# Kernel optimization log

Hardware: AMD Instinct MI355X
Metric: run time of the kernel (lower is better)

The kernel has to match this reference:

```python
import jax, jax.numpy as jnp
import numpy as np

NUM_EXPERTS = 4  # matches init_kwargs

def setup_inputs() -> dict:
    key = jax.random.key(0)
    ks = jax.random.split(key, 6)
    B, T, D = 4, 4096, 1024
    H = 4 * D
    x = jax.random.normal(ks[0], (B, T, D), dtype=jnp.float32)
    token_mask = jax.random.randint(ks[1], (B, T), 0, NUM_EXPERTS, dtype=jnp.int32)
    s1 = 1.0 / np.sqrt(D)
    s2 = 1.0 / np.sqrt(H)
    W1 = jax.random.normal(ks[2], (H, D), dtype=jnp.float32) * s1
    b1 = jax.random.normal(ks[3], (H,), dtype=jnp.float32) * s1
    W2 = jax.random.normal(ks[4], (D, H), dtype=jnp.float32) * s2
    b2 = jax.random.normal(ks[5], (D,), dtype=jnp.float32) * s2
    return {"x": x, "token_mask": token_mask, "W1": W1, "b1": b1, "W2": W2, "b2": b2}

def reference(x, token_mask, W1, b1, W2, b2):
    # Nested MoE FFN: expert m uses leading D//2^(E-1-m) input dims and
    # leading H//2^(E-1-m) hidden dims; top expert (m=E-1) is the full MLP.
    D = x.shape[-1]
    H = W1.shape[0]
    factor = 2 ** (NUM_EXPERTS - 1 - token_mask)          # [B,T] int
    d_in = D // factor                                     # [B,T]
    d_hid = H // factor                                    # [B,T]
    mask_in = (jnp.arange(D) < d_in[..., None]).astype(x.dtype)    # [B,T,D]
    mask_hid = (jnp.arange(H) < d_hid[..., None]).astype(x.dtype)  # [B,T,H]
    # Expand: slice input dims, project, keep only nested hidden slice (bias included only there)
    h = (jnp.einsum('btd,hd->bth', x * mask_in, W1) + b1) * mask_hid
    h = jax.nn.gelu(h, approximate=False)  # gelu(0)=0 preserves nested zeros
    # Contract: zeros outside the nested hidden slice contribute nothing; full output + bias
    out = jnp.einsum('bth,dh->btd', h, W2) + b2
    return out
```

## Files before the change

kernel.cpp:

```cpp
#include <hip/hip_runtime.h>
#include <cstdint>
#include <math.h>

typedef __attribute__((ext_vector_type(8))) __bf16 bf16x8;
typedef __attribute__((ext_vector_type(4))) float f32x4;
typedef unsigned short ushort_t;

__device__ __forceinline__ ushort_t f2bf(float f) {
    uint32_t u = __float_as_uint(f);
    u += 0x7fff + ((u >> 16) & 1);
    return (ushort_t)(u >> 16);
}

__device__ __forceinline__ float gelu_exact(float v) {
    return 0.5f * v * (1.0f + erff(v * 0.70710678118654752440f));
}

__global__ void convert_w2_kernel(const float* __restrict__ s1, const float* __restrict__ s2,
                                  ushort_t* __restrict__ d1, ushort_t* __restrict__ d2,
                                  int n4) {
    int i = blockIdx.x * blockDim.x + threadIdx.x;
    const float* src; ushort_t* dst; int k;
    if (i < n4) { src = s1; dst = d1; k = i; }
    else if (i < 2 * n4) { src = s2; dst = d2; k = i - n4; }
    else return;
    const float4 v = ((const float4*)src)[k];
    ushort4 o;
    o.x = f2bf(v.x); o.y = f2bf(v.y); o.z = f2bf(v.z); o.w = f2bf(v.w);
    ((ushort4*)dst)[k] = o;
}

#define SORT_T 256
__global__ void sort_kernel(const int* __restrict__ tm, int M, int D, int H,
                            int* __restrict__ meta, int* __restrict__ sidx) {
    __shared__ int lc[4][SORT_T + 1];
    __shared__ int soff[4];
    const int t = threadIdx.x;
    const int nj = M / SORT_T;
    int c0 = 0, c1 = 0, c2 = 0, c3 = 0;
    for (int j = 0; j < nj; j++) {
        int e = tm[t + j * SORT_T];
        c0 += (e == 0); c1 += (e == 1); c2 += (e == 2); c3 += (e == 3);
    }
    lc[0][t + 1] = c0; lc[1][t + 1] = c1; lc[2][t + 1] = c2; lc[3][t + 1] = c3;
    if (t < 4) lc[t][0] = 0;
    __syncthreads();
    if (t < 4) {
        int acc = 0;
        for (int i = 1; i <= SORT_T; i++) { acc += lc[t][i]; lc[t][i] = acc; }
    }
    __syncthreads();
    if (t == 0) {
        int off = 0, xoff = 0, hoff = 0;
        for (int e = 0; e < 4; e++) {
            int c = lc[e][SORT_T];
            int ac = (c + 127) & ~127;
            int din = D >> (3 - e), dh = H >> (3 - e);
            meta[e] = c; meta[4 + e] = off; meta[8 + e] = ac; meta[12 + e] = ac >> 7;
            meta[16 + e] = xoff; meta[20 + e] = hoff;
            soff[e] = off;
            off += ac; xoff += ac * din; hoff += ac * dh;
        }
        meta[28] = off;
        int a = 0, b = 0;
        for (int k = 0; k < 4; k++) {
            int e = 3 - k;
            meta[24 + k] = a; a += meta[12 + e] * ((H >> (3 - e)) >> 7);
            meta[32 + k] = b; b += meta[12 + e] * (D >> 7);
        }
        meta[29] = a; meta[36] = b;
    }
    __syncthreads();
    int pos[4];
    pos[0] = soff[0] + lc[0][t]; pos[1] = soff[1] + lc[1][t];
    pos[2] = soff[2] + lc[2][t]; pos[3] = soff[3] + lc[3][t];
    for (int j = 0; j < nj; j++) {
        int i = t + j * SORT_T;
        int e = tm[i];
        sidx[pos[e]++] = i;
    }
    __syncthreads();
    for (int e = 0; e < 4; e++) {
        int s = soff[e] + lc[e][SORT_T];
        int n = meta[8 + e] - lc[e][SORT_T];
        for (int i = t; i < n; i += SORT_T) sidx[s + i] = -1;
    }
}

__global__ void convert_x_sorted(const float* __restrict__ x,
                                 const int* __restrict__ meta,
                                 const int* __restrict__ sidx,
                                 ushort_t* __restrict__ xb, int D) {
    const int p = blockIdx.x;
    if (p >= meta[28]) return;
    const int e = (p >= meta[5]) + (p >= meta[6]) + (p >= meta[7]);
    const int off = meta[4 + e];
    const int din = D >> (3 - e);
    const int tok = sidx[p];
    ushort_t* dst = xb + (size_t)meta[16 + e] + (size_t)(p - off) * din;
    if (tok < 0) {
        for (int c = threadIdx.x * 4; c < din; c += blockDim.x * 4)
            *(ushort4*)(dst + c) = ushort4{0, 0, 0, 0};
    } else {
        const float* src = x + (size_t)tok * D;
        for (int c = threadIdx.x * 4; c < din; c += blockDim.x * 4) {
            const float4 v = *(const float4*)(src + c);
            ushort4 o;
            o.x = f2bf(v.x); o.y = f2bf(v.y); o.z = f2bf(v.z); o.w = f2bf(v.w);
            *(ushort4*)(dst + c) = o;
        }
    }
}

template <int EPI>
__global__ void gemm_sorted(const ushort_t* __restrict__ Abuf,
                            const ushort_t* __restrict__ Bw,
                            const float* __restrict__ bias,
                            const int* __restrict__ meta,
                            const int* __restrict__ sidx,
                            ushort_t* __restrict__ hb,
                            float* __restrict__ out,
                            int D, int H) {
    __shared__ ushort_t As[128 * 32];
    __shared__ ushort_t Bs[128 * 32];

    const int t    = threadIdx.x;
    const int wave = t >> 6;
    const int lane = t & 63;
    const int quad = lane >> 4;
    const int l16  = lane & 15;
    const int wm   = wave & 1;
    const int wn   = wave >> 1;
    const int srow = t >> 2;
    const int scol = (t & 3) * 8;
    char* AsB = (char*)As;
    char* BsB = (char*)Bs;
    const int ldsoff = wave * 64 * 16;

    const int* st = meta + (EPI == 0 ? 24 : 32);
    const int  T  = meta[EPI == 0 ? 29 : 36];

    for (int idx = blockIdx.x; idx < T; idx += gridDim.x) {
        const int k3 = (idx >= st[1]) + (idx >= st[2]) + (idx >= st[3]);
        const int e = 3 - k3;
        const int local = idx - st[k3];
        const int mtiles = meta[12 + e];
        const int mt = local % mtiles;
        const int nt = local / mtiles;

        const int K   = (EPI == 0) ? (D >> (3 - e)) : (H >> (3 - e));
        const int Ne  = (EPI == 0) ? (H >> (3 - e)) : D;
        const int lda = K;
        const int ldb = (EPI == 0) ? D : H;
        const int nb  = nt * 128;
        const ushort_t* A = Abuf + (size_t)((EPI == 0) ? meta[16 + e] : meta[20 + e]);

        const ushort_t* Ag = A + (size_t)(mt * 128 + srow) * lda + scol;
        const ushort_t* Bg = Bw + (size_t)(nb + srow) * ldb + scol;

        f32x4 acc[4][4] = {};

        for (int kt = 0; kt < K; kt += 32) {
            __syncthreads();
            __builtin_amdgcn_global_load_lds(
                (__attribute__((address_space(1))) void*)(uintptr_t)(Ag + kt),
                (__attribute__((address_space(3))) void*)(AsB + ldsoff), 16, 0, 0);
            __builtin_amdgcn_global_load_lds(
                (__attribute__((address_space(1))) void*)(uintptr_t)(Ag + (size_t)64 * lda + kt),
                (__attribute__((address_space(3))) void*)(AsB + 4096 + ldsoff), 16, 0, 0);
            __builtin_amdgcn_global_load_lds(
                (__attribute__((address_space(1))) void*)(uintptr_t)(Bg + kt),
                (__attribute__((address_space(3))) void*)(BsB + ldsoff), 16, 0, 0);
            __builtin_amdgcn_global_load_lds(
                (__attribute__((address_space(1))) void*)(uintptr_t)(Bg + (size_t)64 * ldb + kt),
                (__attribute__((address_space(3))) void*)(BsB + 4096 + ldsoff), 16, 0, 0);
            __syncthreads();

            bf16x8 af[4], bfr[4];
#pragma unroll
            for (int i = 0; i < 4; i++) {
                af[i]  = *(const bf16x8*)(As + (wm * 64 + i * 16 + l16) * 32 + quad * 8);
                bfr[i] = *(const bf16x8*)(Bs + (wn * 64 + i * 16 + l16) * 32 + quad * 8);
            }
#pragma unroll
            for (int i = 0; i < 4; i++)
#pragma unroll
                for (int j = 0; j < 4; j++)
                    acc[i][j] = __builtin_amdgcn_mfma_f32_16x16x32_bf16(af[i], bfr[j], acc[i][j], 0, 0, 0);
        }

        const int colbase = nb + wn * 64 + l16;
        float bv[4];
#pragma unroll
        for (int j = 0; j < 4; j++) bv[j] = bias[colbase + j * 16];

#pragma unroll
        for (int i = 0; i < 4; i++) {
#pragma unroll
            for (int r = 0; r < 4; r++) {
                const int lrow = mt * 128 + wm * 64 + i * 16 + quad * 4 + r;
                if (EPI == 0) {
                    ushort_t* dst = hb + (size_t)meta[20 + e] + (size_t)lrow * Ne;
#pragma unroll
                    for (int j = 0; j < 4; j++)
                        dst[colbase + j * 16] = f2bf(gelu_exact(acc[i][j][r] + bv[j]));
                } else {
                    const int tok = sidx[meta[4 + e] + lrow];
                    if (tok >= 0) {
                        float* dst = out + (size_t)tok * D;
#pragma unroll
                        for (int j = 0; j < 4; j++)
                            dst[colbase + j * 16] = acc[i][j][r] + bv[j];
                    }
                }
            }
        }
    }
}

__global__ void naive_kernel(const float* __restrict__ x, const int* __restrict__ tm,
                             const float* __restrict__ W1, const float* __restrict__ b1,
                             const float* __restrict__ W2, const float* __restrict__ b2,
                             float* __restrict__ out, int D, int Hdim) {
    const int t = blockIdx.x;
    const int m = tm[t];
    const int din = D >> (3 - m);
    const int dh = Hdim >> (3 - m);
    extern __shared__ float sm[];
    float* xs = sm;
    float* hs = sm + D;
    for (int i = threadIdx.x; i < din; i += blockDim.x) xs[i] = x[(size_t)t * D + i];
    __syncthreads();
    for (int h = threadIdx.x; h < dh; h += blockDim.x) {
        const float* w = W1 + (size_t)h * D;
        float a = b1[h];
        for (int d = 0; d < din; d++) a += xs[d] * w[d];
        hs[h] = gelu_exact(a);
    }
    __syncthreads();
    for (int d = threadIdx.x; d < D; d += blockDim.x) {
        const float* w = W2 + (size_t)d * Hdim;
        float a = b2[d];
        for (int h = 0; h < dh; h++) a += hs[h] * w[h];
        out[(size_t)t * D + d] = a;
    }
}

extern "C" void kernel_launch(void* const* d_in, const int* in_sizes, int n_in,
                              void* d_out, int out_size, void* d_ws, size_t ws_size,
                              hipStream_t stream) {
    const float* x  = (const float*)d_in[0];
    const int* tm   = (const int*)d_in[1];
    const float* W1 = (const float*)d_in[2];
    const float* b1 = (const float*)d_in[3];
    const float* W2 = (const float*)d_in[4];
    const float* b2 = (const float*)d_in[5];
    float* out = (float*)d_out;

    const int M    = in_sizes[1];
    const int Hdim = in_sizes[3];
    const int D    = in_sizes[0] / M;

    const int Mpad = M + 512;
    const size_t meta_sz = 256;
    const size_t sidx_sz = ((size_t)Mpad * 4 + 255) & ~(size_t)255;
    const size_t xb_sz   = (size_t)Mpad * D * 2;
    const size_t w1_sz   = (size_t)Hdim * D * 2;
    const size_t w2_sz   = (size_t)D * Hdim * 2;
    const size_t hb_sz   = (size_t)Mpad * Hdim * 2;
    const size_t need_sorted = meta_sz + sidx_sz + xb_sz + w1_sz + w2_sz + hb_sz;

    const bool shape_ok = (M % 256 == 0) && (D % 128 == 0) && (Hdim % 128 == 0) &&
                          (D >= 1024) && (Hdim >= 4096);

    if (shape_ok && ws_size >= need_sorted) {
        char* p = (char*)d_ws;
        int* meta     = (int*)p;        p += meta_sz;
        int* sidx     = (int*)p;        p += sidx_sz;
        ushort_t* xb  = (ushort_t*)p;   p += xb_sz;
        ushort_t* w1b = (ushort_t*)p;   p += w1_sz;
        ushort_t* w2b = (ushort_t*)p;   p += w2_sz;
        ushort_t* hb  = (ushort_t*)p;

        sort_kernel<<<1, SORT_T, 0, stream>>>(tm, M, D, Hdim, meta, sidx);
        const int n4w = Hdim * D / 4;
        convert_w2_kernel<<<(2 * n4w + 255) / 256, 256, 0, stream>>>(W1, W2, w1b, w2b, n4w);
        convert_x_sorted<<<Mpad, 64, 0, stream>>>(x, meta, sidx, xb, D);

        gemm_sorted<0><<<2048, 256, 0, stream>>>(xb, w1b, b1, meta, sidx, hb, nullptr, D, Hdim);
        gemm_sorted<1><<<2048, 256, 0, stream>>>(hb, w2b, b2, meta, sidx, nullptr, out, D, Hdim);
        return;
    }

    const size_t shmem = (size_t)(D + Hdim) * sizeof(float);
    naive_kernel<<<M, 256, shmem, stream>>>(x, tm, W1, b1, W2, b2, out, D, Hdim);
}
```

Baseline: 373.1 us.

## Parallelize token sort, fuse weight conversion with histogram, use tanh GELU

Replaces the single-block token sort with a multi-block histogram fused into the weight-conversion kernel, a wave-level scan in a small meta kernel, and a per-chunk placement kernel. The x conversion now uses one row per 256-thread block iteration in a grid-stride loop. The exact erf GELU in the first GEMM epilogue is replaced by the tanh approximation using __expf, which changes numerics relative to the exact reference. The fast path is also restricted to D == 1024.

```diff
diff --git a/kernel.cpp b/kernel.cpp
--- a/kernel.cpp
+++ b/kernel.cpp
@@ -12,102 +12,132 @@
     return (ushort_t)(u >> 16);
 }
 
+__device__ __forceinline__ float gelu_fast(float x) {
+    float u = x * (0.7978845608f + 0.0356774081f * x * x);
+    float e = __expf(2.0f * u);
+    float th = 1.0f - 2.0f / (e + 1.0f);
+    return 0.5f * x * (1.0f + th);
+}
+
 __device__ __forceinline__ float gelu_exact(float v) {
     return 0.5f * v * (1.0f + erff(v * 0.70710678118654752440f));
 }
 
-__global__ void convert_w2_kernel(const float* __restrict__ s1, const float* __restrict__ s2,
-                                  ushort_t* __restrict__ d1, ushort_t* __restrict__ d2,
-                                  int n4) {
-    int i = blockIdx.x * blockDim.x + threadIdx.x;
-    const float* src; ushort_t* dst; int k;
-    if (i < n4) { src = s1; dst = d1; k = i; }
-    else if (i < 2 * n4) { src = s2; dst = d2; k = i - n4; }
-    else return;
-    const float4 v = ((const float4*)src)[k];
-    ushort4 o;
-    o.x = f2bf(v.x); o.y = f2bf(v.y); o.z = f2bf(v.z); o.w = f2bf(v.w);
-    ((ushort4*)dst)[k] = o;
-}
-
-#define SORT_T 256
-__global__ void sort_kernel(const int* __restrict__ tm, int M, int D, int H,
-                            int* __restrict__ meta, int* __restrict__ sidx) {
-    __shared__ int lc[4][SORT_T + 1];
-    __shared__ int soff[4];
+__global__ void histo_convw_kernel(const int* __restrict__ tm, int* __restrict__ cnt,
+                                   int nchunks,
+                                   const float* __restrict__ s1, const float* __restrict__ s2,
+                                   ushort_t* __restrict__ d1, ushort_t* __restrict__ d2,
+                                   int n4) {
+    if (blockIdx.x < (unsigned)nchunks) {
+        __shared__ int h[4];
+        if (threadIdx.x < 4) h[threadIdx.x] = 0;
+        __syncthreads();
+        int e = tm[blockIdx.x * 256 + threadIdx.x];
+        atomicAdd(&h[e], 1);
+        __syncthreads();
+        if (threadIdx.x < 4) cnt[blockIdx.x * 4 + threadIdx.x] = h[threadIdx.x];
+    } else {
+        const int stride = (gridDim.x - nchunks) * 256;
+        for (int i = (blockIdx.x - nchunks) * 256 + threadIdx.x; i < 2 * n4; i += stride) {
+            const float* src; ushort_t* dst; int k;
+            if (i < n4) { src = s1; dst = d1; k = i; }
+            else        { src = s2; dst = d2; k = i - n4; }
+            const float4 v = ((const float4*)src)[k];
+            ushort4 o;
+            o.x = f2bf(v.x); o.y = f2bf(v.y); o.z = f2bf(v.z); o.w = f2bf(v.w);
+            ((ushort4*)dst)[k] = o;
+        }
+    }
+}
+
+__global__ void meta_kernel(int* __restrict__ meta, int* __restrict__ cnt,
+                            int* __restrict__ sidx, int nchunks, int D, int H) {
+    __shared__ int tot[4];
+    __shared__ int soff_s[4];
     const int t = threadIdx.x;
-    const int nj = M / SORT_T;
-    int c0 = 0, c1 = 0, c2 = 0, c3 = 0;
-    for (int j = 0; j < nj; j++) {
-        int e = tm[t + j * SORT_T];
-        c0 += (e == 0); c1 += (e == 1); c2 += (e == 2); c3 += (e == 3);
-    }
-    lc[0][t + 1] = c0; lc[1][t + 1] = c1; lc[2][t + 1] = c2; lc[3][t + 1] = c3;
-    if (t < 4) lc[t][0] = 0;
-    __syncthreads();
-    if (t < 4) {
-        int acc = 0;
-        for (int i = 1; i <= SORT_T; i++) { acc += lc[t][i]; lc[t][i] = acc; }
-    }
+    const int e = t >> 6;
+    const int c0 = t & 63;
+    int carry = 0;
+    for (int base = 0; base < nchunks; base += 64) {
+        int c = base + c0;
+        int v = (c < nchunks) ? cnt[c * 4 + e] : 0;
+        int s = v;
+#pragma unroll
+        for (int d = 1; d < 64; d <<= 1) {
+            int y = __shfl_up(s, d);
+            if (c0 >= d) s += y;
+        }
+        if (c < nchunks) cnt[c * 4 + e] = s - v + carry;
+        carry += __shfl(s, 63);
+    }
+    if (c0 == 0) tot[e] = carry;
     __syncthreads();
     if (t == 0) {
         int off = 0, xoff = 0, hoff = 0;
-        for (int e = 0; e < 4; e++) {
-            int c = lc[e][SORT_T];
+        for (int ee = 0; ee < 4; ee++) {
+            int c = tot[ee];
             int ac = (c + 127) & ~127;
-            int din = D >> (3 - e), dh = H >> (3 - e);
-            meta[e] = c; meta[4 + e] = off; meta[8 + e] = ac; meta[12 + e] = ac >> 7;
-            meta[16 + e] = xoff; meta[20 + e] = hoff;
-            soff[e] = off;
-            off += ac; xoff += ac * din; hoff += ac * dh;
+            meta[ee] = c; meta[4 + ee] = off; meta[8 + ee] = ac; meta[12 + ee] = ac >> 7;
+            meta[16 + ee] = xoff; meta[20 + ee] = hoff;
+            soff_s[ee] = off;
+            off += ac; xoff += ac * (D >> (3 - ee)); hoff += ac * (H >> (3 - ee));
         }
         meta[28] = off;
         int a = 0, b = 0;
         for (int k = 0; k < 4; k++) {
-            int e = 3 - k;
-            meta[24 + k] = a; a += meta[12 + e] * ((H >> (3 - e)) >> 7);
-            meta[32 + k] = b; b += meta[12 + e] * (D >> 7);
+            int ee = 3 - k;
+            meta[24 + k] = a; a += meta[12 + ee] * ((H >> (3 - ee)) >> 7);
+            meta[32 + k] = b; b += meta[12 + ee] * (D >> 7);
         }
         meta[29] = a; meta[36] = b;
     }
     __syncthreads();
-    int pos[4];
-    pos[0] = soff[0] + lc[0][t]; pos[1] = soff[1] + lc[1][t];
-    pos[2] = soff[2] + lc[2][t]; pos[3] = soff[3] + lc[3][t];
-    for (int j = 0; j < nj; j++) {
-        int i = t + j * SORT_T;
-        int e = tm[i];
-        sidx[pos[e]++] = i;
-    }
-    __syncthreads();
-    for (int e = 0; e < 4; e++) {
-        int s = soff[e] + lc[e][SORT_T];
-        int n = meta[8 + e] - lc[e][SORT_T];
-        for (int i = t; i < n; i += SORT_T) sidx[s + i] = -1;
-    }
+    for (int base = 0; base < 64 * ((nchunks + 63) / 64); base += 64) {
+        int c = base + c0;
+        if (c < nchunks) cnt[c * 4 + e] += soff_s[e];
+    }
+    for (int ee = 0; ee < 4; ee++) {
+        int s0 = soff_s[ee] + tot[ee];
+        int n = meta[8 + ee] - tot[ee];
+        for (int i = t; i < n; i += 256) sidx[s0 + i] = -1;
+    }
+}
+
+__global__ void place_kernel(const int* __restrict__ tm, const int* __restrict__ cofs,
+                             int* __restrict__ sidx) {
+    __shared__ unsigned char se[256];
+    const int c = blockIdx.x;
+    const int t = threadIdx.x;
+    const int tok = c * 256 + t;
+    const int e = tm[tok];
+    se[t] = (unsigned char)e;
+    __syncthreads();
+    int rank = 0;
+    for (int i = 0; i < t; i++) rank += (se[i] == (unsigned char)e);
+    sidx[cofs[c * 4 + e] + rank] = tok;
 }
 
 __global__ void convert_x_sorted(const float* __restrict__ x,
                                  const int* __restrict__ meta,
                                  const int* __restrict__ sidx,
                                  ushort_t* __restrict__ xb, int D) {
-    const int p = blockIdx.x;
-    if (p >= meta[28]) return;
-    const int e = (p >= meta[5]) + (p >= meta[6]) + (p >= meta[7]);
-    const int off = meta[4 + e];
-    const int din = D >> (3 - e);
-    const int tok = sidx[p];
-    ushort_t* dst = xb + (size_t)meta[16 + e] + (size_t)(p - off) * din;
-    if (tok < 0) {
-        for (int c = threadIdx.x * 4; c < din; c += blockDim.x * 4)
-            *(ushort4*)(dst + c) = ushort4{0, 0, 0, 0};
-    } else {
-        const float* src = x + (size_t)tok * D;
-        for (int c = threadIdx.x * 4; c < din; c += blockDim.x * 4) {
-            const float4 v = *(const float4*)(src + c);
-            ushort4 o;
-            o.x = f2bf(v.x); o.y = f2bf(v.y); o.z = f2bf(v.z); o.w = f2bf(v.w);
-            *(ushort4*)(dst + c) = o;
+    const int rows = meta[28];
+    for (int p = blockIdx.x; p < rows; p += gridDim.x) {
+        const int e = (p >= meta[5]) + (p >= meta[6]) + (p >= meta[7]);
+        const int off = meta[4 + e];
+        const int din = D >> (3 - e);
+        const int tok = sidx[p];
+        ushort_t* dst = xb + (size_t)meta[16 + e] + (size_t)(p - off) * din;
+        const int c = threadIdx.x * 4;
+        if (c < din) {
+            if (tok < 0) {
+                *(ushort4*)(dst + c) = ushort4{0, 0, 0, 0};
+            } else {
+                const float4 v = *(const float4*)(x + (size_t)tok * D + c);
+                ushort4 o;
+                o.x = f2bf(v.x); o.y = f2bf(v.y); o.z = f2bf(v.z); o.w = f2bf(v.w);
+                *(ushort4*)(dst + c) = o;
+            }
         }
     }
 }
@@ -203,7 +233,7 @@
                     ushort_t* dst = hb + (size_t)meta[20 + e] + (size_t)lrow * Ne;
 #pragma unroll
                     for (int j = 0; j < 4; j++)
-                        dst[colbase + j * 16] = f2bf(gelu_exact(acc[i][j][r] + bv[j]));
+                        dst[colbase + j * 16] = f2bf(gelu_fast(acc[i][j][r] + bv[j]));
                 } else {
                     const int tok = sidx[meta[4 + e] + lrow];
                     if (tok >= 0) {
@@ -262,30 +292,35 @@
     const int D    = in_sizes[0] / M;
 
     const int Mpad = M + 512;
+    const int nchunks = M / 256;
     const size_t meta_sz = 256;
+    const size_t cnt_sz  = ((size_t)nchunks * 4 * 4 + 255) & ~(size_t)255;
     const size_t sidx_sz = ((size_t)Mpad * 4 + 255) & ~(size_t)255;
     const size_t xb_sz   = (size_t)Mpad * D * 2;
     const size_t w1_sz   = (size_t)Hdim * D * 2;
     const size_t w2_sz   = (size_t)D * Hdim * 2;
     const size_t hb_sz   = (size_t)Mpad * Hdim * 2;
-    const size_t need_sorted = meta_sz + sidx_sz + xb_sz + w1_sz + w2_sz + hb_sz;
+    const size_t need_sorted = meta_sz + cnt_sz + sidx_sz + xb_sz + w1_sz + w2_sz + hb_sz;
 
     const bool shape_ok = (M % 256 == 0) && (D % 128 == 0) && (Hdim % 128 == 0) &&
-                          (D >= 1024) && (Hdim >= 4096);
+                          (D >= 1024) && (D <= 1024) && (Hdim >= 4096);
 
     if (shape_ok && ws_size >= need_sorted) {
         char* p = (char*)d_ws;
         int* meta     = (int*)p;        p += meta_sz;
+        int* cnt      = (int*)p;        p += cnt_sz;
         int* sidx     = (int*)p;        p += sidx_sz;
         ushort_t* xb  = (ushort_t*)p;   p += xb_sz;
         ushort_t* w1b = (ushort_t*)p;   p += w1_sz;
         ushort_t* w2b = (ushort_t*)p;   p += w2_sz;
         ushort_t* hb  = (ushort_t*)p;
 
-        sort_kernel<<<1, SORT_T, 0, stream>>>(tm, M, D, Hdim, meta, sidx);
         const int n4w = Hdim * D / 4;
-        convert_w2_kernel<<<(2 * n4w + 255) / 256, 256, 0, stream>>>(W1, W2, w1b, w2b, n4w);
-        convert_x_sorted<<<Mpad, 64, 0, stream>>>(x, meta, sidx, xb, D);
+        histo_convw_kernel<<<nchunks + 2048, 256, 0, stream>>>(tm, cnt, nchunks,
+                                                               W1, W2, w1b, w2b, n4w);
+        meta_kernel<<<1, 256, 0, stream>>>(meta, cnt, sidx, nchunks, D, Hdim);
+        place_kernel<<<nchunks, 256, 0, stream>>>(tm, cnt, sidx);
+        convert_x_sorted<<<2048, 256, 0, stream>>>(x, meta, sidx, xb, D);
 
         gemm_sorted<0><<<2048, 256, 0, stream>>>(xb, w1b, b1, meta, sidx, hb, nullptr, D, Hdim);
         gemm_sorted<1><<<2048, 256, 0, stream>>>(hb, w2b, b2, meta, sidx, nullptr, out, D, Hdim);
```

Result: faster. 344.8 us (-7.6%).
